# Performance work log

Hardware: AMD Instinct MI355X
Metric: run time of the kernel (lower is better)

The kernel has to match this reference:

```python
import jax, jax.numpy as jnp
import numpy as np

K_MAX = 16
SCALE = 1.0 / (32 * 32)


def setup_inputs() -> dict:
    key = jax.random.key(0)
    k1, k2, k3 = jax.random.split(key, 3)
    B, C_in, C_out, H, W = 16, 32, 32, 256, 256
    x = jax.random.normal(k1, (B, C_in, H, W), dtype=jnp.float32)
    weights_real = SCALE * jax.random.normal(k2, (C_in, C_out, K_MAX, K_MAX), dtype=jnp.float32)
    weights_imag = SCALE * jax.random.normal(k3, (C_in, C_out, K_MAX, K_MAX), dtype=jnp.float32)
    return {"x": x, "weights_real": weights_real, "weights_imag": weights_imag}


def reference(x, weights_real, weights_imag):
    B, C, H, W = x.shape
    C_out = weights_real.shape[1]
    k = min(K_MAX, H, W // 2 + 1)
    x_ft = jnp.fft.rfft2(x, norm='ortho')                 # (B, C, H, W//2+1) complex64
    w = (weights_real + 1j * weights_imag)[:, :, :k, :k]  # (C, C_out, k, k)
    # Faithful to original einsum 'bijk,ijkm->bkm' with broadcast over the
    # size-1 i/j slices: sums x_ft over its ROW axis; x_ft's COLUMN index
    # becomes the output-block row index.
    S = jnp.sum(x_ft[:, :, :k, :k], axis=2)               # (B, C, k)  indexed by freq column
    blk = jnp.einsum('bir,iorc->borc', S, w)              # (B, C_out, k, k)
    out_ft = jnp.zeros((B, C_out, H, W // 2 + 1), dtype=x_ft.dtype)
    out_ft = out_ft.at[:, :, :k, :k].set(blk)
    return jnp.fft.irfft2(out_ft, s=(H, W), norm='ortho')
```

## Files before the change

### kernel.cpp

```cpp
#include <hip/hip_runtime.h>
#include <math.h>


#define TWO_PI_OVER_256 0.02454369260617026

__global__ __launch_bounds__(256) void k0_tables(float* __restrict__ tbl)
{
    const int t = threadIdx.x;
    const double a = TWO_PI_OVER_256 * (double)t;
    tbl[t]       = (float)cos(a);
    tbl[256 + t] = (float)sin(a);
}

__global__ __launch_bounds__(256) void k1_partial(
    const float* __restrict__ x, const float* __restrict__ tbl,
    float* __restrict__ s_part)
{
    __shared__ float twc[256], tws[256];
    __shared__ float gre[64], gim[64];
    __shared__ float Pre[4][256], Pim[4][256];
    __shared__ float red_re[16][16], red_im[16][16];

    const int t = threadIdx.x;
    const int blk = blockIdx.x;
    const int bi = blk >> 2, chunk = blk & 3;
    const int y0 = chunk << 6;

    twc[t] = tbl[t];
    tws[t] = tbl[256 + t];
    __syncthreads();
    if (t < 64) {
        const int h = y0 + t;
        float gr = 0.f, gi = 0.f;
        #pragma unroll
        for (int u = 0; u < 16; ++u) {
            const int idx = (u * h) & 255;
            gr += twc[idx];
            gi -= tws[idx];
        }
        gre[t] = gr; gim[t] = gi;
    }
    __syncthreads();

    const float* img = x + (size_t)bi * 65536 + (size_t)y0 * 256;
    const int cg = t & 63, rg = t >> 6;
    float4 pr = {0.f,0.f,0.f,0.f}, pi = {0.f,0.f,0.f,0.f};
    #pragma unroll 4
    for (int k = 0; k < 16; ++k) {
        const int hl = rg + (k << 2);
        const float4 xv = *(const float4*)(img + (hl << 8) + (cg << 2));
        const float gr = gre[hl], gi = gim[hl];
        pr.x += gr * xv.x; pr.y += gr * xv.y; pr.z += gr * xv.z; pr.w += gr * xv.w;
        pi.x += gi * xv.x; pi.y += gi * xv.y; pi.z += gi * xv.z; pi.w += gi * xv.w;
    }
    *(float4*)&Pre[rg][cg << 2] = pr;
    *(float4*)&Pim[rg][cg << 2] = pi;
    __syncthreads();

    {
        const float sr = Pre[0][t] + Pre[1][t] + Pre[2][t] + Pre[3][t];
        const float si = Pim[0][t] + Pim[1][t] + Pim[2][t] + Pim[3][t];
        Pre[0][t] = sr;
        Pim[0][t] = si;
    }
    __syncthreads();

    {
        const int v = t >> 4, j = t & 15;
        const int i0 = (v * j) & 255;
        float c = twc[i0], s = tws[i0];
        const int id = (v << 4) & 255;
        const float cd = twc[id], sd = tws[id];
        float ar = 0.f, ai = 0.f;
        #pragma unroll
        for (int m = 0; m < 16; ++m) {
            const int w = j + (m << 4);
            const float prr = Pre[0][w];
            const float pii = Pim[0][w];
            ar += prr * c + pii * s;
            ai += pii * c - prr * s;
            const float nc = c * cd - s * sd;
            const float ns = s * cd + c * sd;
            c = nc; s = ns;
        }
        red_re[v][j] = ar; red_im[v][j] = ai;
    }
    __syncthreads();
    if (t < 16) {
        const float4* rr4 = (const float4*)&red_re[t][0];
        const float4* ri4 = (const float4*)&red_im[t][0];
        float ar = 0.f, ai = 0.f;
        #pragma unroll
        for (int q = 0; q < 4; ++q) {
            const float4 a = rr4[q], b = ri4[q];
            ar += a.x + a.y + a.z + a.w;
            ai += b.x + b.y + b.z + b.w;
        }
        float* sp = s_part + (size_t)bi * 128 + chunk * 32;
        sp[t]      = ar * (1.0f / 256.0f);
        sp[t + 16] = ai * (1.0f / 256.0f);
    }
}

__global__ __launch_bounds__(256) void k23_synth(
    const float* __restrict__ wr, const float* __restrict__ wi,
    const float* __restrict__ s_part, const float* __restrict__ tbl,
    float* __restrict__ out)
{
    __shared__ float twc[256], tws[256];
    __shared__ float Sre[32][16], Sim[32][16];
    __shared__ float Btr[16 * 20], Bti[16 * 20];
    __shared__ __align__(16) float coef[64][36];

    const int t = threadIdx.x;
    const int blk = blockIdx.x;
    const int bo = blk >> 2;
    const int y0 = (blk & 3) << 6;
    const int b = bo >> 5, o = bo & 31;

    twc[t] = tbl[t];
    tws[t] = tbl[256 + t];
    {
        const float* sb = s_part + (size_t)b * 4096;
        #pragma unroll
        for (int e = t; e < 512; e += 256) {
            const int i = e >> 4, u = e & 15;
            const float* p = sb + i * 128 + u;
            Sre[i][u] = p[0] + p[32] + p[64] + p[96];
            Sim[i][u] = p[16] + p[48] + p[80] + p[112];
        }
    }
    __syncthreads();

    {
        const int u = t >> 4, v = t & 15;
        float br = 0.f, bim = 0.f;
        const float* wrp = wr + o * 256 + t;
        const float* wip = wi + o * 256 + t;
        #pragma unroll 8
        for (int i = 0; i < 32; ++i) {
            const float a_re = Sre[i][u], a_im = Sim[i][u];
            const float w_re = wrp[i * 8192], w_im = wip[i * 8192];
            br  += a_re * w_re - a_im * w_im;
            bim += a_re * w_im + a_im * w_re;
        }
        Btr[v * 20 + u] = br;
        Bti[v * 20 + u] = bim;
    }
    __syncthreads();

    {
        const int v = t & 15, slot = t >> 4;
        float br[16], bim[16];
        const float4* bpr = (const float4*)&Btr[v * 20];
        const float4* bpi = (const float4*)&Bti[v * 20];
        #pragma unroll
        for (int q = 0; q < 4; ++q) {
            const float4 r4 = bpr[q], i4 = bpi[q];
            br[q*4+0]  = r4.x; br[q*4+1]  = r4.y; br[q*4+2]  = r4.z; br[q*4+3]  = r4.w;
            bim[q*4+0] = i4.x; bim[q*4+1] = i4.y; bim[q*4+2] = i4.z; bim[q*4+3] = i4.w;
        }
        const float scale = (v == 0) ? (1.0f / 256.0f) : (1.0f / 128.0f);
        #pragma unroll
        for (int m = 0; m < 4; ++m) {
            const int r = slot * 4 + m;
            const int y = y0 + r;
            const float c1 = twc[y], s1 = tws[y];
            float gr = br[0], gi = bim[0];
            float cc = 1.f, cs = 0.f;
            #pragma unroll
            for (int u = 1; u < 16; ++u) {
                const float nc = cc * c1 - cs * s1;
                const float ns = cc * s1 + cs * c1;
                cc = nc; cs = ns;
                gr += br[u] * cc - bim[u] * cs;
                gi += br[u] * cs + bim[u] * cc;
            }
            coef[r][v]      = gr * scale;
            coef[r][16 + v] = (v == 0) ? 0.f : (-gi * scale);
        }
    }
    __syncthreads();

    const int c0 = t & 63, rg = t >> 6;
    float cv[16], sv[16];
    #pragma unroll
    for (int v = 0; v < 16; ++v) {
        const int idx = (v * c0) & 255;
        cv[v] = twc[idx];
        sv[v] = tws[idx];
    }
    sv[0] = 0.f;

#define PTERM(ACC, C_, S_, vv) ACC += (C_) * cv[vv] + (S_) * sv[vv];
#define QTERM(ACC, C_, S_, vv) ACC += (S_) * cv[vv] - (C_) * sv[vv];

    float* op = out + (size_t)bo * 65536 + (size_t)y0 * 256 + c0;
    #pragma unroll 2
    for (int rr = 0; rr < 16; ++rr) {
        const int r = (rg << 4) + rr;
        const float4* crow = (const float4*)&coef[r][0];
        const float4 pc0 = crow[0], pc1 = crow[1], pc2 = crow[2], pc3 = crow[3];
        const float4 ps0 = crow[4], ps1 = crow[5], ps2 = crow[6], ps3 = crow[7];
        float P0 = 0.f, P1 = 0.f, P2 = 0.f, P3 = 0.f, Q1 = 0.f, Q3 = 0.f;
        PTERM(P0, pc0.x, ps0.x, 0)
        PTERM(P1, pc0.y, ps0.y, 1)   QTERM(Q1, pc0.y, ps0.y, 1)
        PTERM(P2, pc0.z, ps0.z, 2)
        PTERM(P3, pc0.w, ps0.w, 3)   QTERM(Q3, pc0.w, ps0.w, 3)
        PTERM(P0, pc1.x, ps1.x, 4)
        PTERM(P1, pc1.y, ps1.y, 5)   QTERM(Q1, pc1.y, ps1.y, 5)
        PTERM(P2, pc1.z, ps1.z, 6)
        PTERM(P3, pc1.w, ps1.w, 7)   QTERM(Q3, pc1.w, ps1.w, 7)
        PTERM(P0, pc2.x, ps2.x, 8)
        PTERM(P1, pc2.y, ps2.y, 9)   QTERM(Q1, pc2.y, ps2.y, 9)
        PTERM(P2, pc2.z, ps2.z, 10)
        PTERM(P3, pc2.w, ps2.w, 11)  QTERM(Q3, pc2.w, ps2.w, 11)
        PTERM(P0, pc3.x, ps3.x, 12)
        PTERM(P1, pc3.y, ps3.y, 13)  QTERM(Q1, pc3.y, ps3.y, 13)
        PTERM(P2, pc3.z, ps3.z, 14)
        PTERM(P3, pc3.w, ps3.w, 15)  QTERM(Q3, pc3.w, ps3.w, 15)

        const float e02 = P0 + P2, o13 = P1 + P3;
        const float d02 = P0 - P2, dq  = Q1 - Q3;
        float* row = op + (r << 8);
        __builtin_nontemporal_store(e02 + o13, row);
        __builtin_nontemporal_store(d02 + dq,  row + 64);
        __builtin_nontemporal_store(e02 - o13, row + 128);
        __builtin_nontemporal_store(d02 - dq,  row + 192);
    }
#undef PTERM
#undef QTERM
}

extern "C" void kernel_launch(void* const* d_in, const int* in_sizes, int n_in,
                              void* d_out, int out_size, void* d_ws, size_t ws_size,
                              hipStream_t stream) {
    (void)in_sizes; (void)n_in; (void)out_size; (void)ws_size;
    const float* x  = (const float*)d_in[0];
    const float* wr = (const float*)d_in[1];
    const float* wi = (const float*)d_in[2];
    float* out    = (float*)d_out;
    float* s_part = (float*)d_ws;
    float* tbl    = s_part + 65536;

    k0_tables<<<1, 256, 0, stream>>>(tbl);
    k1_partial<<<2048, 256, 0, stream>>>(x, tbl, s_part);
    k23_synth<<<2048, 256, 0, stream>>>(wr, wi, s_part, tbl, out);
}
```

Measured before the change: 249.0 us.

## Use bf16x3 split MFMA for inverse column DFT synthesis in k23_synth

Replaces the scalar FMA column-synthesis stage, which used folded radix-4 symmetry, with MFMA 16x16x32 bf16 matrix multiplies. Both coefficients and twiddles are split into hi and lo bf16 parts, and three products are summed to keep close to fp32 accuracy. The k0 kernel now precomputes a swizzled bf16 twiddle table laid out for the MFMA B operand. The aim is to move the per-output-pixel arithmetic onto matrix cores, at the cost of an extra table and some precision loss from the three-term split.

New measurement: 255.9 us. 2.8% more time.

```diff
diff --git a/kernel.cpp b/kernel.cpp
--- a/kernel.cpp
+++ b/kernel.cpp
@@ -4,12 +4,52 @@
 
 #define TWO_PI_OVER_256 0.02454369260617026
 
-__global__ __launch_bounds__(256) void k0_tables(float* __restrict__ tbl)
+typedef __attribute__((ext_vector_type(8))) short short8;
+typedef __attribute__((ext_vector_type(4))) float f32x4;
+
+static __device__ inline void bf16split(unsigned short* h, unsigned short* l, float a)
+{
+    const unsigned u = __builtin_bit_cast(unsigned, a);
+    const unsigned short hs = (unsigned short)(u >> 16);
+    *h = hs;
+    const float fh = __builtin_bit_cast(float, (unsigned)hs << 16);
+    const float lo = a - fh;
+    *l = (unsigned short)(__builtin_bit_cast(unsigned, lo) >> 16);
+}
+
+__global__ __launch_bounds__(256) void k0_tables(float* __restrict__ tbl,
+                                                 unsigned short* __restrict__ tswz)
 {
     const int t = threadIdx.x;
-    const double a = TWO_PI_OVER_256 * (double)t;
-    tbl[t]       = (float)cos(a);
-    tbl[256 + t] = (float)sin(a);
+    const int blk = blockIdx.x;
+    if (blk == 0) {
+        const double a = TWO_PI_OVER_256 * (double)t;
+        tbl[t]       = (float)cos(a);
+        tbl[256 + t] = (float)sin(a);
+        return;
+    }
+    const int ct = blk - 1;
+    for (int e = t; e < 1024; e += 256) {
+        const int term = e >> 9;
+        const int lane = (e >> 3) & 63;
+        const int j = e & 7;
+        const int k = ((lane >> 4) << 3) + j;
+        const int x = (ct << 4) + (lane & 15);
+        const int v = (k < 16) ? k : (k - 16);
+        const double ang = TWO_PI_OVER_256 * (double)((v * x) & 255);
+        const float val = (float)((k < 16) ? cos(ang) : sin(ang));
+        const unsigned ubits = __builtin_bit_cast(unsigned, val);
+        const unsigned short hi = (unsigned short)(ubits >> 16);
+        unsigned short wbits;
+        if (term == 0) {
+            wbits = hi;
+        } else {
+            const float fhi = __builtin_bit_cast(float, (unsigned)hi << 16);
+            const float lo = val - fhi;
+            wbits = (unsigned short)(__builtin_bit_cast(unsigned, lo) >> 16);
+        }
+        tswz[((term * 16 + ct) * 64 + lane) * 8 + j] = wbits;
+    }
 }
 
 __global__ __launch_bounds__(256) void k1_partial(
@@ -105,12 +145,13 @@
 __global__ __launch_bounds__(256) void k23_synth(
     const float* __restrict__ wr, const float* __restrict__ wi,
     const float* __restrict__ s_part, const float* __restrict__ tbl,
+    const unsigned short* __restrict__ tswz,
     float* __restrict__ out)
 {
     __shared__ float twc[256], tws[256];
     __shared__ float Sre[32][16], Sim[32][16];
     __shared__ float Btr[16 * 20], Bti[16 * 20];
-    __shared__ __align__(16) float coef[64][36];
+    __shared__ __align__(16) unsigned short Ah[64 * 40], Al[64 * 40];
 
     const int t = threadIdx.x;
     const int blk = blockIdx.x;
@@ -176,60 +217,43 @@
                 gr += br[u] * cc - bim[u] * cs;
                 gi += br[u] * cs + bim[u] * cc;
             }
-            coef[r][v]      = gr * scale;
-            coef[r][16 + v] = (v == 0) ? 0.f : (-gi * scale);
-        }
-    }
-    __syncthreads();
-
-    const int c0 = t & 63, rg = t >> 6;
-    float cv[16], sv[16];
-    #pragma unroll
-    for (int v = 0; v < 16; ++v) {
-        const int idx = (v * c0) & 255;
-        cv[v] = twc[idx];
-        sv[v] = tws[idx];
-    }
-    sv[0] = 0.f;
-
-#define PTERM(ACC, C_, S_, vv) ACC += (C_) * cv[vv] + (S_) * sv[vv];
-#define QTERM(ACC, C_, S_, vv) ACC += (S_) * cv[vv] - (C_) * sv[vv];
-
-    float* op = out + (size_t)bo * 65536 + (size_t)y0 * 256 + c0;
-    #pragma unroll 2
-    for (int rr = 0; rr < 16; ++rr) {
-        const int r = (rg << 4) + rr;
-        const float4* crow = (const float4*)&coef[r][0];
-        const float4 pc0 = crow[0], pc1 = crow[1], pc2 = crow[2], pc3 = crow[3];
-        const float4 ps0 = crow[4], ps1 = crow[5], ps2 = crow[6], ps3 = crow[7];
-        float P0 = 0.f, P1 = 0.f, P2 = 0.f, P3 = 0.f, Q1 = 0.f, Q3 = 0.f;
-        PTERM(P0, pc0.x, ps0.x, 0)
-        PTERM(P1, pc0.y, ps0.y, 1)   QTERM(Q1, pc0.y, ps0.y, 1)
-        PTERM(P2, pc0.z, ps0.z, 2)
-        PTERM(P3, pc0.w, ps0.w, 3)   QTERM(Q3, pc0.w, ps0.w, 3)
-        PTERM(P0, pc1.x, ps1.x, 4)
-        PTERM(P1, pc1.y, ps1.y, 5)   QTERM(Q1, pc1.y, ps1.y, 5)
-        PTERM(P2, pc1.z, ps1.z, 6)
-        PTERM(P3, pc1.w, ps1.w, 7)   QTERM(Q3, pc1.w, ps1.w, 7)
-        PTERM(P0, pc2.x, ps2.x, 8)
-        PTERM(P1, pc2.y, ps2.y, 9)   QTERM(Q1, pc2.y, ps2.y, 9)
-        PTERM(P2, pc2.z, ps2.z, 10)
-        PTERM(P3, pc2.w, ps2.w, 11)  QTERM(Q3, pc2.w, ps2.w, 11)
-        PTERM(P0, pc3.x, ps3.x, 12)
-        PTERM(P1, pc3.y, ps3.y, 13)  QTERM(Q1, pc3.y, ps3.y, 13)
-        PTERM(P2, pc3.z, ps3.z, 14)
-        PTERM(P3, pc3.w, ps3.w, 15)  QTERM(Q3, pc3.w, ps3.w, 15)
-
-        const float e02 = P0 + P2, o13 = P1 + P3;
-        const float d02 = P0 - P2, dq  = Q1 - Q3;
-        float* row = op + (r << 8);
-        __builtin_nontemporal_store(e02 + o13, row);
-        __builtin_nontemporal_store(d02 + dq,  row + 64);
-        __builtin_nontemporal_store(e02 - o13, row + 128);
-        __builtin_nontemporal_store(d02 - dq,  row + 192);
-    }
-#undef PTERM
-#undef QTERM
+            const float a0 = gr * scale;
+            const float a1 = (v == 0) ? 0.f : (-gi * scale);
+            bf16split(&Ah[r * 40 + v],      &Al[r * 40 + v],      a0);
+            bf16split(&Ah[r * 40 + 16 + v], &Al[r * 40 + 16 + v], a1);
+        }
+    }
+    __syncthreads();
+
+    {
+        const int lane = t & 63, wv = t >> 6;
+        short8 afh[4], afl[4];
+        #pragma unroll
+        for (int m = 0; m < 4; ++m) {
+            const int off = (m * 16 + (lane & 15)) * 40 + ((lane >> 4) << 3);
+            afh[m] = *(const short8*)&Ah[off];
+            afl[m] = *(const short8*)&Al[off];
+        }
+        float* outb = out + (size_t)bo * 65536 + (size_t)y0 * 256;
+        #pragma unroll
+        for (int q = 0; q < 4; ++q) {
+            const int ct = (wv << 2) + q;
+            const short8 bh = *(const short8*)&tswz[(size_t)(ct * 64 + lane) * 8];
+            const short8 bl = *(const short8*)&tswz[(size_t)((16 + ct) * 64 + lane) * 8];
+            #pragma unroll
+            for (int m = 0; m < 4; ++m) {
+                f32x4 acc = {0.f, 0.f, 0.f, 0.f};
+                acc = __builtin_amdgcn_mfma_f32_16x16x32_bf16(afh[m], bh, acc, 0, 0, 0);
+                acc = __builtin_amdgcn_mfma_f32_16x16x32_bf16(afh[m], bl, acc, 0, 0, 0);
+                acc = __builtin_amdgcn_mfma_f32_16x16x32_bf16(afl[m], bh, acc, 0, 0, 0);
+                float* op = outb + (size_t)(16 * m + ((lane >> 4) << 2)) * 256
+                                 + (ct << 4) + (lane & 15);
+                #pragma unroll
+                for (int reg = 0; reg < 4; ++reg)
+                    __builtin_nontemporal_store(acc[reg], op + reg * 256);
+            }
+        }
+    }
 }
 
 extern "C" void kernel_launch(void* const* d_in, const int* in_sizes, int n_in,
@@ -242,8 +266,9 @@
     float* out    = (float*)d_out;
     float* s_part = (float*)d_ws;
     float* tbl    = s_part + 65536;
-
-    k0_tables<<<1, 256, 0, stream>>>(tbl);
+    unsigned short* tswz = (unsigned short*)(tbl + 512);
+
+    k0_tables<<<17, 256, 0, stream>>>(tbl, tswz);
     k1_partial<<<2048, 256, 0, stream>>>(x, tbl, s_part);
-    k23_synth<<<2048, 256, 0, stream>>>(wr, wi, s_part, tbl, out);
-}
+    k23_synth<<<2048, 256, 0, stream>>>(wr, wi, s_part, tbl, tswz, out);
+}
```
